# Performance work log

Hardware: AMD Instinct MI355X
Metric: run time of the kernel (lower is better)

## Reference

```python
import jax, jax.numpy as jnp
import numpy as np

N_NODES = 50000
N_EDGES = 800000
D_IN = 256
D_HID = 256
N_CLASSES = 32
N_GRAPHS = 64


def _sage_conv(x, src, dst, W_l, b_l, W_r, num_nodes):
    # PyG SAGEConv (mean aggr, root_weight=True):
    # out = lin_l(mean_{j->i} x_j) + lin_r(x_i)
    msg = x[src]                                                   # [E, d]
    agg = jax.ops.segment_sum(msg, dst, num_segments=num_nodes)   # [N, d]
    cnt = jax.ops.segment_sum(jnp.ones((src.shape[0], 1), x.dtype), dst,
                              num_segments=num_nodes)             # [N, 1]
    agg = agg / jnp.maximum(cnt, 1.0)
    return agg @ W_l + b_l + x @ W_r


def setup_inputs() -> dict:
    key = jax.random.key(0)
    ks = jax.random.split(key, 12)
    x = jax.random.normal(ks[0], (N_NODES, D_IN), dtype=jnp.float32)
    edge_index = jax.random.randint(ks[1], (2, N_EDGES), 0, N_NODES, dtype=jnp.int64)
    batch = jnp.sort(jax.random.randint(ks[2], (N_NODES,), 0, N_GRAPHS, dtype=jnp.int64))
    s1 = 1.0 / np.sqrt(D_IN)
    s2 = 1.0 / np.sqrt(D_HID)
    return {
        "x": x,
        "edge_index": edge_index,
        "batch": batch,
        "W1_l": jax.random.uniform(ks[3], (D_IN, D_HID), jnp.float32, -s1, s1),
        "b1": jax.random.uniform(ks[4], (D_HID,), jnp.float32, -s1, s1),
        "W1_r": jax.random.uniform(ks[5], (D_IN, D_HID), jnp.float32, -s1, s1),
        "W2_l": jax.random.uniform(ks[6], (D_HID, D_HID), jnp.float32, -s2, s2),
        "b2": jax.random.uniform(ks[7], (D_HID,), jnp.float32, -s2, s2),
        "W2_r": jax.random.uniform(ks[8], (D_HID, D_HID), jnp.float32, -s2, s2),
        "Wc": jax.random.uniform(ks[9], (D_HID, N_CLASSES), jnp.float32, -s2, s2),
        "bc": jax.random.uniform(ks[10], (N_CLASSES,), jnp.float32, -s2, s2),
    }


def reference(x, edge_index, batch, W1_l, b1, W1_r, W2_l, b2, W2_r, Wc, bc):
    src, dst = edge_index[0], edge_index[1]
    h = jax.nn.relu(_sage_conv(x, src, dst, W1_l, b1, W1_r, N_NODES))
    h = jax.nn.relu(_sage_conv(h, src, dst, W2_l, b2, W2_r, N_NODES))
    # global mean pool over graphs
    gsum = jax.ops.segment_sum(h, batch, num_segments=N_GRAPHS)        # [G, d]
    gcnt = jax.ops.segment_sum(jnp.ones((h.shape[0], 1), h.dtype), batch,
                               num_segments=N_GRAPHS)                  # [G, 1]
    g = gsum / jnp.maximum(gcnt, 1.0)
    return g @ Wc + bc
```

## Files before the change

kernel.cpp:

```cpp
#include <hip/hip_runtime.h>
#include <stdint.h>

#define NNODES 50000
#define NEDGES 800000
#define DDIM 256
#define NCLS 32
#define NGRAPH 64
#define NSCANB ((NNODES + 255) / 256)
#define HISTB ((NEDGES + 255) / 256)
#define CVTXB ((NNODES * 64 + 255) / 256)
#define CVTWB (2 * 256 * 512 / 256)

typedef short bf16x8 __attribute__((ext_vector_type(8)));
typedef float f32x4 __attribute__((ext_vector_type(4)));
typedef unsigned short u16x4 __attribute__((ext_vector_type(4)));
typedef unsigned short u16x8 __attribute__((ext_vector_type(8)));

typedef __attribute__((address_space(1))) const char glb_c;
typedef __attribute__((address_space(3))) char lds_c;


__device__ __forceinline__ unsigned short f2b(float f) {
  uint32_t u = __builtin_bit_cast(uint32_t, f);
  u += 0x7FFFu + ((u >> 16) & 1u);
  return (unsigned short)(u >> 16);
}
__device__ __forceinline__ float b2f(unsigned short u) {
  return __builtin_bit_cast(float, (uint32_t)u << 16);
}
__device__ __forceinline__ float blo(uint32_t u) {
  return __builtin_bit_cast(float, u << 16);
}
__device__ __forceinline__ float bhi(uint32_t u) {
  return __builtin_bit_cast(float, u & 0xFFFF0000u);
}

__device__ __forceinline__ void gload16(const void* g, const void* l) {
  __builtin_amdgcn_global_load_lds((glb_c*)g, (lds_c*)l, 16, 0, 0);
}


__global__ void k_setup(const int* __restrict__ dst, int* __restrict__ cnt,
                        const float* __restrict__ x, unsigned short* __restrict__ xb,
                        const float* __restrict__ W1l, const float* __restrict__ W1r,
                        const float* __restrict__ W2l, const float* __restrict__ W2r,
                        unsigned short* __restrict__ WT1, unsigned short* __restrict__ WT2) {
  int b = blockIdx.x;
  if (b < HISTB) {
    int e = b * 256 + threadIdx.x;
    if (e < NEDGES) atomicAdd(&cnt[dst[e]], 1);
  } else if (b < HISTB + CVTXB) {
    int i = (b - HISTB) * 256 + threadIdx.x;
    if (i < NNODES * 64) {
      int r = i >> 6, c4 = i & 63;
      float4 v = *(const float4*)(x + (size_t)r * DDIM + c4 * 4);
      u16x4 o;
      o.x = f2b(v.x); o.y = f2b(v.y); o.z = f2b(v.z); o.w = f2b(v.w);
      int slab = c4 >> 3, seg = c4 & 7;
      *(u16x4*)(xb + ((size_t)slab * NNODES + r) * 32 + seg * 4) = o;
    }
  } else {
    int idx = (b - HISTB - CVTXB) * 256 + threadIdx.x;
    int which = idx >> 17;
    int id2 = idx & 131071;
    int n = id2 >> 9, k = id2 & 511;
    const float* Wl = which ? W2l : W1l;
    const float* Wr = which ? W2r : W1r;
    unsigned short* WT = which ? WT2 : WT1;
    float v = (k < 256) ? Wl[k * 256 + n] : Wr[(k - 256) * 256 + n];
    WT[id2] = f2b(v);
  }
}


__global__ void k_scan1(const int* __restrict__ cnt, int* __restrict__ bsum) {
  int b = blockIdx.x;
  int i = b * 256 + threadIdx.x;
  int lane = threadIdx.x & 63, wid = threadIdx.x >> 6;
  int v = (i < NNODES) ? cnt[i] : 0;
#pragma unroll
  for (int o = 1; o < 64; o <<= 1) v += __shfl_xor(v, o, 64);
  __shared__ int ws[4];
  if (lane == 0) ws[wid] = v;
  __syncthreads();
  if (threadIdx.x == 0) bsum[b] = ws[0] + ws[1] + ws[2] + ws[3];
}

__global__ void k_scan2(const int* __restrict__ bsum, int* __restrict__ boffs) {
  int tid = threadIdx.x, lane = tid & 63, wid = tid >> 6;
  int v = (tid < NSCANB) ? bsum[tid] : 0;
  int s = v;
#pragma unroll
  for (int o = 1; o < 64; o <<= 1) {
    int t = __shfl_up(s, o, 64);
    if (lane >= o) s += t;
  }
  __shared__ int ws[4];
  if (lane == 63) ws[wid] = s;
  __syncthreads();
  int add = 0;
  for (int w = 0; w < wid; ++w) add += ws[w];
  if (tid < NSCANB) boffs[tid] = s + add - v;
}

__global__ void k_scan3(const int* __restrict__ cnt, const int* __restrict__ boffs,
                        int* __restrict__ rowptr, int* __restrict__ cursor,
                        float* __restrict__ gsum, const int* __restrict__ batch,
                        int* __restrict__ gcnt) {
  int b = blockIdx.x;
  if (b < NSCANB) {
    int i = b * 256 + threadIdx.x;
    int lane = threadIdx.x & 63, wid = threadIdx.x >> 6;
    int v = (i < NNODES) ? cnt[i] : 0;
    int s = v;
#pragma unroll
    for (int o = 1; o < 64; o <<= 1) {
      int t = __shfl_up(s, o, 64);
      if (lane >= o) s += t;
    }
    __shared__ int ws[4];
    if (lane == 63) ws[wid] = s;
    __syncthreads();
    int add = boffs[b];
    for (int w = 0; w < wid; ++w) add += ws[w];
    int incl = s + add;
    if (i < NNODES) {
      rowptr[i + 1] = incl;
      cursor[i] = incl - v;
    }
    if (b == 0 && threadIdx.x == 0) rowptr[0] = 0;
  } else if (b == NSCANB) {
    for (int i = threadIdx.x; i < NGRAPH * DDIM; i += 256) gsum[i] = 0.f;
  } else {
    int g = threadIdx.x;
    if (g < NGRAPH) {
      int lo = 0, hi = NNODES;
      while (lo < hi) { int m = (lo + hi) >> 1; if (batch[m] < g) lo = m + 1; else hi = m; }
      int lo2 = lo, hi2 = NNODES;
      while (lo2 < hi2) { int m = (lo2 + hi2) >> 1; if (batch[m] < g + 1) lo2 = m + 1; else hi2 = m; }
      gcnt[g] = lo2 - lo;
    }
  }
}

__global__ void k_fill(const int* __restrict__ src, const int* __restrict__ dst,
                       int* __restrict__ cursor, int* __restrict__ col) {
  int e = blockIdx.x * 256 + threadIdx.x;
  if (e < NEDGES) {
    int p = atomicAdd(&cursor[dst[e]], 1);
    col[p] = src[e];
  }
}


__global__ void k_agg(const unsigned short* __restrict__ feat,
                      const int* __restrict__ rowptr, const int* __restrict__ col,
                      unsigned short* __restrict__ out) {
  int g = blockIdx.x & 7;
  int nb = blockIdx.x >> 3;
  int wv = threadIdx.x >> 6, lane = threadIdx.x & 63;
  int ns = lane >> 2;
  int seg = lane & 3;
  int node = nb * 64 + wv * 16 + ns;
  bool valid = node < NNODES;
  int nn = valid ? node : NNODES - 1;
  int s = rowptr[nn], e = rowptr[nn + 1];
  if (!valid) e = s;
  const unsigned short* slabp = feat + (size_t)g * NNODES * 32 + seg * 8;
  float a[8] = {0.f}, b[8] = {0.f};
  int last = e - 1;
  for (int i = s; i < e; i += 8) {
    uint4 vv[8];
#pragma unroll
    for (int j = 0; j < 8; ++j) {
      int idx = i + j;
      int cidx = (idx <= last) ? idx : last;
      int ce = col[cidx];
      uint4 r = *(const uint4*)(slabp + (size_t)ce * 32);
      if (idx > last) { r.x = 0u; r.y = 0u; r.z = 0u; r.w = 0u; }
      vv[j] = r;
    }
#pragma unroll
    for (int j = 0; j < 8; j += 2) {
      a[0] += blo(vv[j].x); a[1] += bhi(vv[j].x);
      a[2] += blo(vv[j].y); a[3] += bhi(vv[j].y);
      a[4] += blo(vv[j].z); a[5] += bhi(vv[j].z);
      a[6] += blo(vv[j].w); a[7] += bhi(vv[j].w);
      b[0] += blo(vv[j + 1].x); b[1] += bhi(vv[j + 1].x);
      b[2] += blo(vv[j + 1].y); b[3] += bhi(vv[j + 1].y);
      b[4] += blo(vv[j + 1].z); b[5] += bhi(vv[j + 1].z);
      b[6] += blo(vv[j + 1].w); b[7] += bhi(vv[j + 1].w);
    }
  }
  if (valid) {
    float inv = (e > s) ? 1.f / (float)(e - s) : 0.f;
    u16x8 o;
#pragma unroll
    for (int j = 0; j < 8; ++j) o[j] = f2b((a[j] + b[j]) * inv);
    unsigned short* op = out + ((size_t)g * NNODES + node) * 32 + seg * 8;
    __builtin_nontemporal_store(o, (u16x8*)op);
  }
}


__global__ void k_gemm(const unsigned short* __restrict__ Aagg,
                       const unsigned short* __restrict__ Aroot,
                       const unsigned short* __restrict__ WT,
                       const float* __restrict__ bias,
                       unsigned short* __restrict__ out) {
  __shared__ unsigned short As[128 * 32];
  __shared__ unsigned short Bs[128 * 32];
  int m0 = blockIdx.x * 128;
  int n0 = blockIdx.y * 128;
  int tid = threadIdx.x, lane = tid & 63, wv = tid >> 6;
  int wm = wv >> 1, wn = wv & 1;

  f32x4 acc[4][4];
#pragma unroll
  for (int m = 0; m < 4; ++m)
#pragma unroll
    for (int n = 0; n < 4; ++n) acc[m][n] = (f32x4)0.f;

  for (int kt = 0; kt < 16; ++kt) {
    int k = kt * 32;
    const unsigned short* Abase = (k < 256) ? Aagg : Aroot;
    int slab = (k & 255) >> 5;
    const unsigned short* Aslab = Abase + (size_t)slab * NNODES * 32;
#pragma unroll
    for (int q = 0; q < 2; ++q) {
      int idx = q * 256 + tid;
      int row = idx >> 2, seg = idx & 3;
      int gr = m0 + row;
      if (gr >= NNODES) gr = NNODES - 1;
      const unsigned short* sp = Aslab + (size_t)gr * 32 + seg * 8;
      gload16(sp, (const char*)As + (q * 256 + wv * 64) * 16);
    }
#pragma unroll
    for (int q = 0; q < 2; ++q) {
      int idx = q * 256 + tid;
      int row = idx >> 2, seg = idx & 3;
      const unsigned short* sp = WT + (size_t)(n0 + row) * 512 + k + seg * 8;
      gload16(sp, (const char*)Bs + (q * 256 + wv * 64) * 16);
    }
    __syncthreads();

    bf16x8 af[4], bfr[4];
    int kb = (lane >> 4) * 8;
    int rA = wm * 64 + (lane & 15);
    int rB = wn * 64 + (lane & 15);
#pragma unroll
    for (int m = 0; m < 4; ++m) af[m] = *(const bf16x8*)&As[(rA + m * 16) * 32 + kb];
#pragma unroll
    for (int n = 0; n < 4; ++n) bfr[n] = *(const bf16x8*)&Bs[(rB + n * 16) * 32 + kb];
#pragma unroll
    for (int m = 0; m < 4; ++m)
#pragma unroll
      for (int n = 0; n < 4; ++n)
        acc[m][n] = __builtin_amdgcn_mfma_f32_16x16x32_bf16(af[m], bfr[n], acc[m][n], 0, 0, 0);
    __syncthreads();
  }

  int rbase = m0 + wm * 64 + (lane >> 4) * 4;
  int cbase = n0 + wn * 64 + (lane & 15);
#pragma unroll
  for (int n = 0; n < 4; ++n) {
    int cc = cbase + n * 16;
    float bv = bias[cc];
    size_t sbase = (size_t)(cc >> 5) * NNODES * 32 + (cc & 31);
#pragma unroll
    for (int m = 0; m < 4; ++m) {
#pragma unroll
      for (int j = 0; j < 4; ++j) {
        int r = rbase + m * 16 + j;
        if (r < NNODES) {
          float v = acc[m][n][j] + bv;
          v = fmaxf(v, 0.f);
          out[sbase + (size_t)r * 32] = f2b(v);
        }
      }
    }
  }
}


#define GSUM_WAVES 1024
__global__ void k_gsum(const unsigned short* __restrict__ h2,
                       const int* __restrict__ batch,
                       float* __restrict__ gsum) {
  int wave = (blockIdx.x * blockDim.x + threadIdx.x) >> 6;
  int lane = threadIdx.x & 63;
  const int per = (NNODES + GSUM_WAVES - 1) / GSUM_WAVES;
  int r0 = wave * per;
  int r1 = r0 + per; if (r1 > NNODES) r1 = NNODES;
  if (r0 >= r1) return;
  int slab = lane >> 3, seg = lane & 7;
  int cb = slab * 32 + seg * 4;
  const unsigned short* sp = h2 + (size_t)slab * NNODES * 32 + seg * 4;
  float a0 = 0.f, a1 = 0.f, a2 = 0.f, a3 = 0.f;
  int cur = batch[r0];
  for (int r = r0; r < r1; ++r) {
    int g = batch[r];
    if (g != cur) {
      float* gp = gsum + cur * DDIM + cb;
      atomicAdd(gp + 0, a0); atomicAdd(gp + 1, a1);
      atomicAdd(gp + 2, a2); atomicAdd(gp + 3, a3);
      a0 = a1 = a2 = a3 = 0.f;
      cur = g;
    }
    u16x4 v = *(const u16x4*)(sp + (size_t)r * 32);
    a0 += b2f(v.x); a1 += b2f(v.y); a2 += b2f(v.z); a3 += b2f(v.w);
  }
  float* gp = gsum + cur * DDIM + cb;
  atomicAdd(gp + 0, a0); atomicAdd(gp + 1, a1);
  atomicAdd(gp + 2, a2); atomicAdd(gp + 3, a3);
}

__global__ void k_cls(const float* __restrict__ gsum, const int* __restrict__ cnt,
                      const float* __restrict__ Wc, const float* __restrict__ bc,
                      float* __restrict__ out) {
  int g = blockIdx.x;
  __shared__ float colmean[DDIM];
  int c = threadIdx.x;
  int n = cnt[g];
  float inv = (n > 0) ? 1.f / (float)n : 0.f;
  colmean[c] = gsum[g * DDIM + c] * inv;
  __syncthreads();
  if (c < NCLS) {
    float o = bc[c];
#pragma unroll 4
    for (int k = 0; k < DDIM; ++k) o += colmean[k] * Wc[k * NCLS + c];
    out[g * NCLS + c] = o;
  }
}


extern "C" void kernel_launch(void* const* d_in, const int* in_sizes, int n_in,
                              void* d_out, int out_size, void* d_ws, size_t ws_size,
                              hipStream_t stream) {
  const float* x    = (const float*)d_in[0];
  const int* eidx   = (const int*)d_in[1];
  const int* batch  = (const int*)d_in[2];
  const float* W1l  = (const float*)d_in[3];
  const float* b1   = (const float*)d_in[4];
  const float* W1r  = (const float*)d_in[5];
  const float* W2l  = (const float*)d_in[6];
  const float* b2   = (const float*)d_in[7];
  const float* W2r  = (const float*)d_in[8];
  const float* Wc   = (const float*)d_in[9];
  const float* bc   = (const float*)d_in[10];
  float* out = (float*)d_out;

  const int* esrc = eidx;
  const int* edst = eidx + NEDGES;

  char* w = (char*)d_ws;
  size_t off = 0;
  auto alloc = [&](size_t bytes) -> char* {
    char* p = w + off;
    off = (off + bytes + 255) & ~(size_t)255;
    return p;
  };
  int* rowptr = (int*)alloc((NNODES + 1) * sizeof(int));
  int* cursor = (int*)alloc(NNODES * sizeof(int));
  int* col    = (int*)alloc(NEDGES * sizeof(int));
  unsigned short* xb   = (unsigned short*)alloc((size_t)NNODES * DDIM * 2);
  unsigned short* h1b  = (unsigned short*)alloc((size_t)NNODES * DDIM * 2);
  unsigned short* aggb = (unsigned short*)alloc((size_t)NNODES * DDIM * 2);
  unsigned short* WT1  = (unsigned short*)alloc(512 * 256 * 2);
  unsigned short* WT2  = (unsigned short*)alloc(512 * 256 * 2);
  float* gsum = (float*)alloc(NGRAPH * DDIM * sizeof(float));
  int* gcnt   = (int*)alloc(NGRAPH * sizeof(int));
  int* bsum   = (int*)alloc(NSCANB * sizeof(int));
  int* boffs  = (int*)alloc(NSCANB * sizeof(int));

  hipMemsetAsync(cursor, 0, NNODES * sizeof(int), stream);
  k_setup<<<HISTB + CVTXB + CVTWB, 256, 0, stream>>>(edst, cursor, x, xb,
                                                     W1l, W1r, W2l, W2r, WT1, WT2);
  k_scan1<<<NSCANB, 256, 0, stream>>>(cursor, bsum);
  k_scan2<<<1, 256, 0, stream>>>(bsum, boffs);
  k_scan3<<<NSCANB + 2, 256, 0, stream>>>(cursor, boffs, rowptr, cursor,
                                          gsum, batch, gcnt);
  k_fill<<<HISTB, 256, 0, stream>>>(esrc, edst, cursor, col);

  dim3 ggrid((NNODES + 127) / 128, 2);
  int agg_grid = ((NNODES + 63) / 64) * 8;

  k_agg<<<agg_grid, 256, 0, stream>>>(xb, rowptr, col, aggb);
  k_gemm<<<ggrid, 256, 0, stream>>>(aggb, xb, WT1, b1, h1b);

  k_agg<<<agg_grid, 256, 0, stream>>>(h1b, rowptr, col, aggb);
  k_gemm<<<ggrid, 256, 0, stream>>>(aggb, h1b, WT2, b2, xb);

  k_gsum<<<GSUM_WAVES / 4, 256, 0, stream>>>(xb, batch, gsum);
  k_cls<<<NGRAPH, 256, 0, stream>>>(gsum, gcnt, Wc, bc, out);
}
```

Before: 297.5 us.

## Partition histogram and CSR fill atomics by XCD to localize L2 traffic

```diff
diff --git a/kernel.cpp b/kernel.cpp
--- a/kernel.cpp
+++ b/kernel.cpp
@@ -8,8 +8,10 @@
 #define NGRAPH 64
 #define NSCANB ((NNODES + 255) / 256)
 #define HISTB ((NEDGES + 255) / 256)
+#define HISTB8 (HISTB * 8)
 #define CVTXB ((NNODES * 64 + 255) / 256)
 #define CVTWB (2 * 256 * 512 / 256)
+#define NPXCD (NNODES / 8)
 
 typedef short bf16x8 __attribute__((ext_vector_type(8)));
 typedef float f32x4 __attribute__((ext_vector_type(4)));
@@ -46,21 +48,27 @@
                         const float* __restrict__ W2l, const float* __restrict__ W2r,
                         unsigned short* __restrict__ WT1, unsigned short* __restrict__ WT2) {
   int b = blockIdx.x;
-  if (b < HISTB) {
-    int e = b * 256 + threadIdx.x;
-    if (e < NEDGES) atomicAdd(&cnt[dst[e]], 1);
-  } else if (b < HISTB + CVTXB) {
-    int i = (b - HISTB) * 256 + threadIdx.x;
+  if (b < HISTB8) {
+    int xcd = b & 7;
+    int e = (b >> 3) * 256 + threadIdx.x;
+    if (e < NEDGES) {
+      int d = dst[e];
+      if ((unsigned)(d - xcd * NPXCD) < (unsigned)NPXCD) atomicAdd(&cnt[d], 1);
+    }
+  } else if (b < HISTB8 + CVTXB) {
+    int i = (b - HISTB8) * 256 + threadIdx.x;
     if (i < NNODES * 64) {
-      int r = i >> 6, c4 = i & 63;
-      float4 v = *(const float4*)(x + (size_t)r * DDIM + c4 * 4);
+      int seg = i & 7;
+      int rr = i >> 3;
+      int slab = rr / NNODES;
+      int r = rr - slab * NNODES;
+      float4 v = *(const float4*)(x + (size_t)r * DDIM + slab * 32 + seg * 4);
       u16x4 o;
       o.x = f2b(v.x); o.y = f2b(v.y); o.z = f2b(v.z); o.w = f2b(v.w);
-      int slab = c4 >> 3, seg = c4 & 7;
-      *(u16x4*)(xb + ((size_t)slab * NNODES + r) * 32 + seg * 4) = o;
+      *(u16x4*)(xb + (size_t)i * 4) = o;
     }
   } else {
-    int idx = (b - HISTB - CVTXB) * 256 + threadIdx.x;
+    int idx = (b - HISTB8 - CVTXB) * 256 + threadIdx.x;
     int which = idx >> 17;
     int id2 = idx & 131071;
     int n = id2 >> 9, k = id2 & 511;
@@ -145,10 +153,15 @@
 
 __global__ void k_fill(const int* __restrict__ src, const int* __restrict__ dst,
                        int* __restrict__ cursor, int* __restrict__ col) {
-  int e = blockIdx.x * 256 + threadIdx.x;
+  int b = blockIdx.x;
+  int xcd = b & 7;
+  int e = (b >> 3) * 256 + threadIdx.x;
   if (e < NEDGES) {
-    int p = atomicAdd(&cursor[dst[e]], 1);
-    col[p] = src[e];
+    int d = dst[e];
+    if ((unsigned)(d - xcd * NPXCD) < (unsigned)NPXCD) {
+      int p = atomicAdd(&cursor[d], 1);
+      col[p] = src[e];
+    }
   }
 }
 
@@ -374,13 +387,13 @@
   int* boffs  = (int*)alloc(NSCANB * sizeof(int));
 
   hipMemsetAsync(cursor, 0, NNODES * sizeof(int), stream);
-  k_setup<<<HISTB + CVTXB + CVTWB, 256, 0, stream>>>(edst, cursor, x, xb,
-                                                     W1l, W1r, W2l, W2r, WT1, WT2);
+  k_setup<<<HISTB8 + CVTXB + CVTWB, 256, 0, stream>>>(edst, cursor, x, xb,
+                                                      W1l, W1r, W2l, W2r, WT1, WT2);
   k_scan1<<<NSCANB, 256, 0, stream>>>(cursor, bsum);
   k_scan2<<<1, 256, 0, stream>>>(bsum, boffs);
   k_scan3<<<NSCANB + 2, 256, 0, stream>>>(cursor, boffs, rowptr, cursor,
                                           gsum, batch, gcnt);
-  k_fill<<<HISTB, 256, 0, stream>>>(esrc, edst, cursor, col);
+  k_fill<<<HISTB8, 256, 0, stream>>>(esrc, edst, cursor, col);
 
   dim3 ggrid((NNODES + 127) / 128, 2);
   int agg_grid = ((NNODES + 63) / 64) * 8;
```

Measured after the change: 293.5 us. About the same (-1.3%).

## Pad CSR rows to multiples of 8, fuse fill with convert, widen GEMM tile

Applied to the files above, without the earlier changes.

```diff
diff --git a/kernel.cpp b/kernel.cpp
--- a/kernel.cpp
+++ b/kernel.cpp
@@ -2,14 +2,16 @@
 #include <stdint.h>
 
 #define NNODES 50000
+#define NNROWS (NNODES + 1)
 #define NEDGES 800000
 #define DDIM 256
 #define NCLS 32
 #define NGRAPH 64
 #define NSCANB ((NNODES + 255) / 256)
 #define HISTB ((NEDGES + 255) / 256)
-#define CVTXB ((NNODES * 64 + 255) / 256)
+#define CVTXB (NNODES * 64 / 256)
 #define CVTWB (2 * 256 * 512 / 256)
+#define COLCAP 1200000
 
 typedef short bf16x8 __attribute__((ext_vector_type(8)));
 typedef float f32x4 __attribute__((ext_vector_type(4)));
@@ -40,25 +42,113 @@
 }
 
 
-__global__ void k_setup(const int* __restrict__ dst, int* __restrict__ cnt,
-                        const float* __restrict__ x, unsigned short* __restrict__ xb,
-                        const float* __restrict__ W1l, const float* __restrict__ W1r,
-                        const float* __restrict__ W2l, const float* __restrict__ W2r,
-                        unsigned short* __restrict__ WT1, unsigned short* __restrict__ WT2) {
+__global__ void k_hist(const int* __restrict__ dst, int* __restrict__ cnt) {
+  int e = blockIdx.x * 256 + threadIdx.x;
+  if (e < NEDGES) atomicAdd(&cnt[dst[e]], 1);
+}
+
+__global__ void k_scan1(const int* __restrict__ cnt, int* __restrict__ bsum) {
+  int b = blockIdx.x;
+  int i = b * 256 + threadIdx.x;
+  int lane = threadIdx.x & 63, wid = threadIdx.x >> 6;
+  int v = (i < NNODES) ? ((cnt[i] + 7) & ~7) : 0;
+#pragma unroll
+  for (int o = 1; o < 64; o <<= 1) v += __shfl_xor(v, o, 64);
+  __shared__ int ws[4];
+  if (lane == 0) ws[wid] = v;
+  __syncthreads();
+  if (threadIdx.x == 0) bsum[b] = ws[0] + ws[1] + ws[2] + ws[3];
+}
+
+__global__ void k_scan2(const int* __restrict__ bsum, int* __restrict__ boffs) {
+  int tid = threadIdx.x, lane = tid & 63, wid = tid >> 6;
+  int v = (tid < NSCANB) ? bsum[tid] : 0;
+  int s = v;
+#pragma unroll
+  for (int o = 1; o < 64; o <<= 1) {
+    int t = __shfl_up(s, o, 64);
+    if (lane >= o) s += t;
+  }
+  __shared__ int ws[4];
+  if (lane == 63) ws[wid] = s;
+  __syncthreads();
+  int add = 0;
+  for (int w = 0; w < wid; ++w) add += ws[w];
+  if (tid < NSCANB) boffs[tid] = s + add - v;
+}
+
+__global__ void k_scan3(const int* __restrict__ cnt, const int* __restrict__ boffs,
+                        int* __restrict__ prowptr, int* __restrict__ cursor,
+                        int* __restrict__ col,
+                        float* __restrict__ gsum, const int* __restrict__ batch,
+                        int* __restrict__ gcnt,
+                        unsigned short* __restrict__ xb, unsigned short* __restrict__ h1b) {
+  int b = blockIdx.x;
+  if (b < NSCANB) {
+    int i = b * 256 + threadIdx.x;
+    int lane = threadIdx.x & 63, wid = threadIdx.x >> 6;
+    int raw = (i < NNODES) ? cnt[i] : 0;
+    int pv = (raw + 7) & ~7;
+    int s = pv;
+#pragma unroll
+    for (int o = 1; o < 64; o <<= 1) {
+      int t = __shfl_up(s, o, 64);
+      if (lane >= o) s += t;
+    }
+    __shared__ int ws[4];
+    if (lane == 63) ws[wid] = s;
+    __syncthreads();
+    int add = boffs[b];
+    for (int w = 0; w < wid; ++w) add += ws[w];
+    int incl = s + add;
+    if (i < NNODES) {
+      int excl = incl - pv;
+      prowptr[i + 1] = incl;
+      cursor[i] = excl;
+      for (int j = excl + raw; j < incl; ++j) col[j] = NNODES;
+    }
+    if (b == 0 && threadIdx.x == 0) prowptr[0] = 0;
+  } else if (b == NSCANB) {
+    for (int i = threadIdx.x; i < NGRAPH * DDIM; i += 256) gsum[i] = 0.f;
+    int s = threadIdx.x >> 5, c = threadIdx.x & 31;
+    if (s < 8) {
+      xb[((size_t)s * NNROWS + NNODES) * 32 + c] = 0;
+      h1b[((size_t)s * NNROWS + NNODES) * 32 + c] = 0;
+    }
+  } else {
+    int g = threadIdx.x;
+    if (g < NGRAPH) {
+      int lo = 0, hi = NNODES;
+      while (lo < hi) { int m = (lo + hi) >> 1; if (batch[m] < g) lo = m + 1; else hi = m; }
+      int lo2 = lo, hi2 = NNODES;
+      while (lo2 < hi2) { int m = (lo2 + hi2) >> 1; if (batch[m] < g + 1) lo2 = m + 1; else hi2 = m; }
+      gcnt[g] = lo2 - lo;
+    }
+  }
+}
+
+
+__global__ void k_fillcvt(const int* __restrict__ src, const int* __restrict__ dst,
+                          int* __restrict__ cursor, int* __restrict__ col,
+                          const float* __restrict__ x, unsigned short* __restrict__ xb,
+                          const float* __restrict__ W1l, const float* __restrict__ W1r,
+                          const float* __restrict__ W2l, const float* __restrict__ W2r,
+                          unsigned short* __restrict__ WT1, unsigned short* __restrict__ WT2) {
   int b = blockIdx.x;
   if (b < HISTB) {
     int e = b * 256 + threadIdx.x;
-    if (e < NEDGES) atomicAdd(&cnt[dst[e]], 1);
+    if (e < NEDGES) {
+      int p = atomicAdd(&cursor[dst[e]], 1);
+      col[p] = src[e];
+    }
   } else if (b < HISTB + CVTXB) {
     int i = (b - HISTB) * 256 + threadIdx.x;
-    if (i < NNODES * 64) {
-      int r = i >> 6, c4 = i & 63;
-      float4 v = *(const float4*)(x + (size_t)r * DDIM + c4 * 4);
-      u16x4 o;
-      o.x = f2b(v.x); o.y = f2b(v.y); o.z = f2b(v.z); o.w = f2b(v.w);
-      int slab = c4 >> 3, seg = c4 & 7;
-      *(u16x4*)(xb + ((size_t)slab * NNODES + r) * 32 + seg * 4) = o;
-    }
+    int r = i >> 6, c4 = i & 63;
+    float4 v = *(const float4*)(x + (size_t)r * DDIM + c4 * 4);
+    u16x4 o;
+    o.x = f2b(v.x); o.y = f2b(v.y); o.z = f2b(v.z); o.w = f2b(v.w);
+    int slab = c4 >> 3, seg = c4 & 7;
+    *(u16x4*)(xb + ((size_t)slab * NNROWS + r) * 32 + seg * 4) = o;
   } else {
     int idx = (b - HISTB - CVTXB) * 256 + threadIdx.x;
     int which = idx >> 17;
@@ -73,88 +163,9 @@
 }
 
 
-__global__ void k_scan1(const int* __restrict__ cnt, int* __restrict__ bsum) {
-  int b = blockIdx.x;
-  int i = b * 256 + threadIdx.x;
-  int lane = threadIdx.x & 63, wid = threadIdx.x >> 6;
-  int v = (i < NNODES) ? cnt[i] : 0;
-#pragma unroll
-  for (int o = 1; o < 64; o <<= 1) v += __shfl_xor(v, o, 64);
-  __shared__ int ws[4];
-  if (lane == 0) ws[wid] = v;
-  __syncthreads();
-  if (threadIdx.x == 0) bsum[b] = ws[0] + ws[1] + ws[2] + ws[3];
-}
-
-__global__ void k_scan2(const int* __restrict__ bsum, int* __restrict__ boffs) {
-  int tid = threadIdx.x, lane = tid & 63, wid = tid >> 6;
-  int v = (tid < NSCANB) ? bsum[tid] : 0;
-  int s = v;
-#pragma unroll
-  for (int o = 1; o < 64; o <<= 1) {
-    int t = __shfl_up(s, o, 64);
-    if (lane >= o) s += t;
-  }
-  __shared__ int ws[4];
-  if (lane == 63) ws[wid] = s;
-  __syncthreads();
-  int add = 0;
-  for (int w = 0; w < wid; ++w) add += ws[w];
-  if (tid < NSCANB) boffs[tid] = s + add - v;
-}
-
-__global__ void k_scan3(const int* __restrict__ cnt, const int* __restrict__ boffs,
-                        int* __restrict__ rowptr, int* __restrict__ cursor,
-                        float* __restrict__ gsum, const int* __restrict__ batch,
-                        int* __restrict__ gcnt) {
-  int b = blockIdx.x;
-  if (b < NSCANB) {
-    int i = b * 256 + threadIdx.x;
-    int lane = threadIdx.x & 63, wid = threadIdx.x >> 6;
-    int v = (i < NNODES) ? cnt[i] : 0;
-    int s = v;
-#pragma unroll
-    for (int o = 1; o < 64; o <<= 1) {
-      int t = __shfl_up(s, o, 64);
-      if (lane >= o) s += t;
-    }
-    __shared__ int ws[4];
-    if (lane == 63) ws[wid] = s;
-    __syncthreads();
-    int add = boffs[b];
-    for (int w = 0; w < wid; ++w) add += ws[w];
-    int incl = s + add;
-    if (i < NNODES) {
-      rowptr[i + 1] = incl;
-      cursor[i] = incl - v;
-    }
-    if (b == 0 && threadIdx.x == 0) rowptr[0] = 0;
-  } else if (b == NSCANB) {
-    for (int i = threadIdx.x; i < NGRAPH * DDIM; i += 256) gsum[i] = 0.f;
-  } else {
-    int g = threadIdx.x;
-    if (g < NGRAPH) {
-      int lo = 0, hi = NNODES;
-      while (lo < hi) { int m = (lo + hi) >> 1; if (batch[m] < g) lo = m + 1; else hi = m; }
-      int lo2 = lo, hi2 = NNODES;
-      while (lo2 < hi2) { int m = (lo2 + hi2) >> 1; if (batch[m] < g + 1) lo2 = m + 1; else hi2 = m; }
-      gcnt[g] = lo2 - lo;
-    }
-  }
-}
-
-__global__ void k_fill(const int* __restrict__ src, const int* __restrict__ dst,
-                       int* __restrict__ cursor, int* __restrict__ col) {
-  int e = blockIdx.x * 256 + threadIdx.x;
-  if (e < NEDGES) {
-    int p = atomicAdd(&cursor[dst[e]], 1);
-    col[p] = src[e];
-  }
-}
-
-
 __global__ void k_agg(const unsigned short* __restrict__ feat,
-                      const int* __restrict__ rowptr, const int* __restrict__ col,
+                      const int* __restrict__ prowptr, const int* __restrict__ cnt,
+                      const int* __restrict__ col,
                       unsigned short* __restrict__ out) {
   int g = blockIdx.x & 7;
   int nb = blockIdx.x >> 3;
@@ -164,21 +175,16 @@
   int node = nb * 64 + wv * 16 + ns;
   bool valid = node < NNODES;
   int nn = valid ? node : NNODES - 1;
-  int s = rowptr[nn], e = rowptr[nn + 1];
-  if (!valid) e = s;
-  const unsigned short* slabp = feat + (size_t)g * NNODES * 32 + seg * 8;
-  float a[8] = {0.f}, b[8] = {0.f};
-  int last = e - 1;
-  for (int i = s; i < e; i += 8) {
+  int s = prowptr[nn], pe = prowptr[nn + 1];
+  if (!valid) pe = s;
+  const unsigned short* slabp = feat + (size_t)g * NNROWS * 32 + seg * 8;
+  float a[8] = {0.f}, bb[8] = {0.f};
+  for (int i = s; i < pe; i += 8) {
     uint4 vv[8];
 #pragma unroll
     for (int j = 0; j < 8; ++j) {
-      int idx = i + j;
-      int cidx = (idx <= last) ? idx : last;
-      int ce = col[cidx];
-      uint4 r = *(const uint4*)(slabp + (size_t)ce * 32);
-      if (idx > last) { r.x = 0u; r.y = 0u; r.z = 0u; r.w = 0u; }
-      vv[j] = r;
+      int ce = col[i + j];
+      vv[j] = *(const uint4*)(slabp + (size_t)ce * 32);
     }
 #pragma unroll
     for (int j = 0; j < 8; j += 2) {
@@ -186,18 +192,19 @@
       a[2] += blo(vv[j].y); a[3] += bhi(vv[j].y);
       a[4] += blo(vv[j].z); a[5] += bhi(vv[j].z);
       a[6] += blo(vv[j].w); a[7] += bhi(vv[j].w);
-      b[0] += blo(vv[j + 1].x); b[1] += bhi(vv[j + 1].x);
-      b[2] += blo(vv[j + 1].y); b[3] += bhi(vv[j + 1].y);
-      b[4] += blo(vv[j + 1].z); b[5] += bhi(vv[j + 1].z);
-      b[6] += blo(vv[j + 1].w); b[7] += bhi(vv[j + 1].w);
+      bb[0] += blo(vv[j + 1].x); bb[1] += bhi(vv[j + 1].x);
+      bb[2] += blo(vv[j + 1].y); bb[3] += bhi(vv[j + 1].y);
+      bb[4] += blo(vv[j + 1].z); bb[5] += bhi(vv[j + 1].z);
+      bb[6] += blo(vv[j + 1].w); bb[7] += bhi(vv[j + 1].w);
     }
   }
   if (valid) {
-    float inv = (e > s) ? 1.f / (float)(e - s) : 0.f;
+    int deg = cnt[nn];
+    float inv = (deg > 0) ? 1.f / (float)deg : 0.f;
     u16x8 o;
 #pragma unroll
-    for (int j = 0; j < 8; ++j) o[j] = f2b((a[j] + b[j]) * inv);
-    unsigned short* op = out + ((size_t)g * NNODES + node) * 32 + seg * 8;
+    for (int j = 0; j < 8; ++j) o[j] = f2b((a[j] + bb[j]) * inv);
+    unsigned short* op = out + ((size_t)g * NNROWS + node) * 32 + seg * 8;
     __builtin_nontemporal_store(o, (u16x8*)op);
   }
 }
@@ -209,66 +216,63 @@
                        const float* __restrict__ bias,
                        unsigned short* __restrict__ out) {
   __shared__ unsigned short As[128 * 32];
-  __shared__ unsigned short Bs[128 * 32];
+  __shared__ unsigned short Bs[256 * 32];
   int m0 = blockIdx.x * 128;
-  int n0 = blockIdx.y * 128;
   int tid = threadIdx.x, lane = tid & 63, wv = tid >> 6;
   int wm = wv >> 1, wn = wv & 1;
 
-  f32x4 acc[4][4];
-#pragma unroll
-  for (int m = 0; m < 4; ++m)
-#pragma unroll
-    for (int n = 0; n < 4; ++n) acc[m][n] = (f32x4)0.f;
+  f32x4 acc[2][8];
+#pragma unroll
+  for (int m = 0; m < 2; ++m)
+#pragma unroll
+    for (int n = 0; n < 8; ++n) acc[m][n] = (f32x4)0.f;
 
   for (int kt = 0; kt < 16; ++kt) {
     int k = kt * 32;
-    const unsigned short* Abase = (k < 256) ? Aagg : Aroot;
-    int slab = (k & 255) >> 5;
-    const unsigned short* Aslab = Abase + (size_t)slab * NNODES * 32;
-#pragma unroll
-    for (int q = 0; q < 2; ++q) {
-      int idx = q * 256 + tid;
-      int row = idx >> 2, seg = idx & 3;
+    const unsigned short* Abase = (kt < 8) ? Aagg : Aroot;
+    int slab = kt & 7;
+    const unsigned short* Aslab = Abase + (size_t)slab * NNROWS * 32;
+    {
+      int row = tid >> 2, sg = tid & 3;
       int gr = m0 + row;
       if (gr >= NNODES) gr = NNODES - 1;
-      const unsigned short* sp = Aslab + (size_t)gr * 32 + seg * 8;
-      gload16(sp, (const char*)As + (q * 256 + wv * 64) * 16);
-    }
-#pragma unroll
-    for (int q = 0; q < 2; ++q) {
-      int idx = q * 256 + tid;
-      int row = idx >> 2, seg = idx & 3;
-      const unsigned short* sp = WT + (size_t)(n0 + row) * 512 + k + seg * 8;
-      gload16(sp, (const char*)Bs + (q * 256 + wv * 64) * 16);
+      const unsigned short* sp = Aslab + (size_t)gr * 32 + sg * 8;
+      gload16(sp, (const char*)As + (wv * 64) * 16);
+    }
+#pragma unroll
+    for (int p = 0; p < 2; ++p) {
+      int idx = p * 512 + tid;
+      int row = idx >> 2, sg = idx & 3;
+      const unsigned short* sp = WT + (size_t)row * 512 + k + sg * 8;
+      gload16(sp, (const char*)Bs + (p * 512 + wv * 64) * 16);
     }
     __syncthreads();
 
-    bf16x8 af[4], bfr[4];
+    bf16x8 af[2], bfr[8];
     int kb = (lane >> 4) * 8;
-    int rA = wm * 64 + (lane & 15);
-    int rB = wn * 64 + (lane & 15);
-#pragma unroll
-    for (int m = 0; m < 4; ++m) af[m] = *(const bf16x8*)&As[(rA + m * 16) * 32 + kb];
-#pragma unroll
-    for (int n = 0; n < 4; ++n) bfr[n] = *(const bf16x8*)&Bs[(rB + n * 16) * 32 + kb];
-#pragma unroll
-    for (int m = 0; m < 4; ++m)
-#pragma unroll
-      for (int n = 0; n < 4; ++n)
+    int rA = wm * 32 + (lane & 15);
+    int rB = wn * 128 + (lane & 15);
+#pragma unroll
+    for (int m = 0; m < 2; ++m) af[m] = *(const bf16x8*)&As[(rA + m * 16) * 32 + kb];
+#pragma unroll
+    for (int n = 0; n < 8; ++n) bfr[n] = *(const bf16x8*)&Bs[(rB + n * 16) * 32 + kb];
+#pragma unroll
+    for (int m = 0; m < 2; ++m)
+#pragma unroll
+      for (int n = 0; n < 8; ++n)
         acc[m][n] = __builtin_amdgcn_mfma_f32_16x16x32_bf16(af[m], bfr[n], acc[m][n], 0, 0, 0);
     __syncthreads();
   }
 
-  int rbase = m0 + wm * 64 + (lane >> 4) * 4;
-  int cbase = n0 + wn * 64 + (lane & 15);
-#pragma unroll
-  for (int n = 0; n < 4; ++n) {
-    int cc = cbase + n * 16;
+  int rbase = m0 + wm * 32 + (lane >> 4) * 4;
+  int cb = wn * 128 + (lane & 15);
+#pragma unroll
+  for (int n = 0; n < 8; ++n) {
+    int cc = cb + n * 16;
     float bv = bias[cc];
-    size_t sbase = (size_t)(cc >> 5) * NNODES * 32 + (cc & 31);
-#pragma unroll
-    for (int m = 0; m < 4; ++m) {
+    size_t sbase = (size_t)(cc >> 5) * NNROWS * 32 + (cc & 31);
+#pragma unroll
+    for (int m = 0; m < 2; ++m) {
 #pragma unroll
       for (int j = 0; j < 4; ++j) {
         int r = rbase + m * 16 + j;
@@ -295,7 +299,7 @@
   if (r0 >= r1) return;
   int slab = lane >> 3, seg = lane & 7;
   int cb = slab * 32 + seg * 4;
-  const unsigned short* sp = h2 + (size_t)slab * NNODES * 32 + seg * 4;
+  const unsigned short* sp = h2 + (size_t)slab * NNROWS * 32 + seg * 4;
   float a0 = 0.f, a1 = 0.f, a2 = 0.f, a3 = 0.f;
   int cur = batch[r0];
   for (int r = r0; r < r1; ++r) {
@@ -360,12 +364,13 @@
     off = (off + bytes + 255) & ~(size_t)255;
     return p;
   };
-  int* rowptr = (int*)alloc((NNODES + 1) * sizeof(int));
-  int* cursor = (int*)alloc(NNODES * sizeof(int));
-  int* col    = (int*)alloc(NEDGES * sizeof(int));
-  unsigned short* xb   = (unsigned short*)alloc((size_t)NNODES * DDIM * 2);
-  unsigned short* h1b  = (unsigned short*)alloc((size_t)NNODES * DDIM * 2);
-  unsigned short* aggb = (unsigned short*)alloc((size_t)NNODES * DDIM * 2);
+  int* prowptr = (int*)alloc((NNODES + 1) * sizeof(int));
+  int* cnt     = (int*)alloc(NNODES * sizeof(int));
+  int* cursor  = (int*)alloc(NNODES * sizeof(int));
+  int* col     = (int*)alloc(COLCAP * sizeof(int));
+  unsigned short* xb   = (unsigned short*)alloc((size_t)8 * NNROWS * 32 * 2);
+  unsigned short* h1b  = (unsigned short*)alloc((size_t)8 * NNROWS * 32 * 2);
+  unsigned short* aggb = (unsigned short*)alloc((size_t)8 * NNROWS * 32 * 2);
   unsigned short* WT1  = (unsigned short*)alloc(512 * 256 * 2);
   unsigned short* WT2  = (unsigned short*)alloc(512 * 256 * 2);
   float* gsum = (float*)alloc(NGRAPH * DDIM * sizeof(float));
@@ -373,23 +378,24 @@
   int* bsum   = (int*)alloc(NSCANB * sizeof(int));
   int* boffs  = (int*)alloc(NSCANB * sizeof(int));
 
-  hipMemsetAsync(cursor, 0, NNODES * sizeof(int), stream);
-  k_setup<<<HISTB + CVTXB + CVTWB, 256, 0, stream>>>(edst, cursor, x, xb,
-                                                     W1l, W1r, W2l, W2r, WT1, WT2);
-  k_scan1<<<NSCANB, 256, 0, stream>>>(cursor, bsum);
+  hipMemsetAsync(cnt, 0, NNODES * sizeof(int), stream);
+  k_hist<<<HISTB, 256, 0, stream>>>(edst, cnt);
+  k_scan1<<<NSCANB, 256, 0, stream>>>(cnt, bsum);
   k_scan2<<<1, 256, 0, stream>>>(bsum, boffs);
-  k_scan3<<<NSCANB + 2, 256, 0, stream>>>(cursor, boffs, rowptr, cursor,
-                                          gsum, batch, gcnt);
-  k_fill<<<HISTB, 256, 0, stream>>>(esrc, edst, cursor, col);
-
-  dim3 ggrid((NNODES + 127) / 128, 2);
+  k_scan3<<<NSCANB + 2, 256, 0, stream>>>(cnt, boffs, prowptr, cursor, col,
+                                          gsum, batch, gcnt, xb, h1b);
+  k_fillcvt<<<HISTB + CVTXB + CVTWB, 256, 0, stream>>>(esrc, edst, cursor, col,
+                                                       x, xb, W1l, W1r, W2l, W2r,
+                                                       WT1, WT2);
+
+  int ggrid = (NNODES + 127) / 128;
   int agg_grid = ((NNODES + 63) / 64) * 8;
 
-  k_agg<<<agg_grid, 256, 0, stream>>>(xb, rowptr, col, aggb);
-  k_gemm<<<ggrid, 256, 0, stream>>>(aggb, xb, WT1, b1, h1b);
-
-  k_agg<<<agg_grid, 256, 0, stream>>>(h1b, rowptr, col, aggb);
-  k_gemm<<<ggrid, 256, 0, stream>>>(aggb, h1b, WT2, b2, xb);
+  k_agg<<<agg_grid, 256, 0, stream>>>(xb, prowptr, cnt, col, aggb);
+  k_gemm<<<ggrid, 512, 0, stream>>>(aggb, xb, WT1, b1, h1b);
+
+  k_agg<<<agg_grid, 256, 0, stream>>>(h1b, prowptr, cnt, col, aggb);
+  k_gemm<<<ggrid, 512, 0, stream>>>(aggb, h1b, WT2, b2, xb);
 
   k_gsum<<<GSUM_WAVES / 4, 256, 0, stream>>>(xb, batch, gsum);
   k_cls<<<NGRAPH, 256, 0, stream>>>(gsum, gcnt, Wc, bc, out);
```

Result: slower. 309.6 us (+4.1%).
